# Kernel optimization log

Measured on AMD Instinct MI355X. Metric: run time of the kernel, lower is better.

The kernel has to match this reference:

```python
import jax, jax.numpy as jnp
import numpy as np

B, T, H, W = 32, 20, 64, 64
EPS = 1e-08
SPARSITY_W, CONC_W, FOCAL_ALPHA, COORD_W, BG_W = 0.8, 1.5, 1.0, 1.0, 0.1
GAMMA = 2.0


def setup_inputs() -> dict:
    key = jax.random.key(0)
    k1, k2 = jax.random.split(key)
    predictions = jax.random.normal(k1, (B, T, H, W), dtype=jnp.float32)
    targets = (jax.random.uniform(k2, (B, T, H, W)) < 0.001).astype(jnp.float32)
    return {"predictions": predictions, "targets": targets}


def _loss(pred, tgt):
    p = jax.nn.sigmoid(pred)                       # sigmoid computed once
    # focal loss (stable BCE-with-logits)
    bce = jnp.maximum(pred, 0.0) - pred * tgt + jnp.log1p(jnp.exp(-jnp.abs(pred)))
    p_t = jnp.where(tgt == 1.0, p, 1.0 - p)
    focal = jnp.mean(FOCAL_ALPHA * (1.0 - p_t) ** GAMMA * bce)
    # sparsity: entropy of per-(b,t) normalized map
    pf = p.reshape(B, T, H * W)
    pf_n = pf / (pf.sum(axis=-1, keepdims=True) + EPS)
    sparsity = jnp.mean(-jnp.sum(pf_n * jnp.log(pf_n + EPS), axis=-1))
    # concentration: 1 - max per (b,t)
    concentration = jnp.mean(1.0 - pf.max(axis=-1))
    # soft coordinate loss: center-of-mass distance per (b,t), fully vectorized
    xc = jnp.arange(W, dtype=jnp.float32)
    yc = jnp.arange(H, dtype=jnp.float32)
    ps = p.sum(axis=(-2, -1)) + EPS                 # [B,T]
    ts = tgt.sum(axis=(-2, -1)) + EPS
    px = jnp.einsum('bthw,w->bt', p, xc) / ps
    py = jnp.einsum('bthw,h->bt', p, yc) / ps
    tx = jnp.einsum('bthw,w->bt', tgt, xc) / ts
    ty = jnp.einsum('bthw,h->bt', tgt, yc) / ts
    coordinate = jnp.mean(jnp.sqrt((px - tx) ** 2 + (py - ty) ** 2))
    # background MSE
    background = jnp.mean((p * (tgt == 0.0).astype(p.dtype)) ** 2)
    total = (focal + SPARSITY_W * sparsity + CONC_W * concentration
             + COORD_W * coordinate + BG_W * background)
    return total


def reference(predictions, targets):
    return _loss(predictions, targets)
```

## Files before the change

kernel.cpp:

```cpp
#include <hip/hip_runtime.h>
#include <math.h>

#define B_ 32
#define T_ 20
#define H_ 64
#define W_ 64
#define HW 4096
#define BT 640
#define NTOT 2621440.0f
#define EPS 1e-8f
#define SPARSITY_W 0.8f
#define CONC_W 1.5f
#define COORD_W 1.0f
#define BG_W 0.1f

__global__ __launch_bounds__(256) void k1_stats(
    const float* __restrict__ pred, const float* __restrict__ tgt,
    float* __restrict__ stats)
{
    const int bt = blockIdx.x;
    const float4* p4 = (const float4*)(pred + (size_t)bt * HW);
    const float4* t4 = (const float4*)(tgt  + (size_t)bt * HW);

    float sp = 0.f, st = 0.f, spx = 0.f, spy = 0.f, stx = 0.f, sty = 0.f;
    float foc = 0.f, bg = 0.f, mx = -1e30f;

    for (int f = threadIdx.x; f < HW / 4; f += 256) {
        float4 xv = p4[f];
        float4 tv = t4[f];
        const int pix0 = f * 4;
        const float h  = (float)(pix0 >> 6);
        const float w0 = (float)(pix0 & 63);
        float xs[4] = {xv.x, xv.y, xv.z, xv.w};
        float ts[4] = {tv.x, tv.y, tv.z, tv.w};
#pragma unroll
        for (int k = 0; k < 4; k++) {
            const float x = xs[k];
            const float t = ts[k];
            const float p = 1.f / (1.f + expf(-x));
            const float bce = fmaxf(x, 0.f) - x * t + log1pf(expf(-fabsf(x)));
            const float pt = (t == 1.f) ? p : (1.f - p);
            const float om = 1.f - pt;
            foc += om * om * bce;
            if (t == 0.f) bg += p * p;
            const float w = w0 + (float)k;
            sp  += p;      st  += t;
            spx += p * w;  spy += p * h;
            stx += t * w;  sty += t * h;
            mx = fmaxf(mx, p);
        }
    }

    float vals[9] = {sp, st, spx, spy, stx, sty, foc, bg, mx};
#pragma unroll
    for (int o = 32; o > 0; o >>= 1) {
#pragma unroll
        for (int i = 0; i < 8; i++) vals[i] += __shfl_down(vals[i], o);
        vals[8] = fmaxf(vals[8], __shfl_down(vals[8], o));
    }
    __shared__ float sm[4][9];
    const int lane = threadIdx.x & 63;
    const int wv   = threadIdx.x >> 6;
    if (lane == 0) {
#pragma unroll
        for (int i = 0; i < 9; i++) sm[wv][i] = vals[i];
    }
    __syncthreads();
    if (threadIdx.x == 0) {
        float r[9];
#pragma unroll
        for (int i = 0; i < 9; i++) r[i] = sm[0][i];
        for (int v = 1; v < 4; v++) {
#pragma unroll
            for (int i = 0; i < 8; i++) r[i] += sm[v][i];
            r[8] = fmaxf(r[8], sm[v][8]);
        }
        const float Sp = r[0], St = r[1];
        const float psd = Sp + EPS, tsd = St + EPS;
        const float px = r[2] / psd, py = r[3] / psd;
        const float tx = r[4] / tsd, ty = r[5] / tsd;
        const float dx = px - tx, dy = py - ty;
        const float coord = sqrtf(dx * dx + dy * dy);
        const float contrib =
            r[6] * (1.0f / NTOT)
          + BG_W * r[7] * (1.0f / NTOT)
          + (CONC_W * (1.0f - r[8]) + COORD_W * coord) * (1.0f / (float)BT);
        stats[bt * 2 + 0] = contrib;
        stats[bt * 2 + 1] = Sp;
    }
}

__global__ __launch_bounds__(256) void k2_entropy(
    const float* __restrict__ pred, const float* __restrict__ stats,
    float* __restrict__ out)
{
    const int bt = blockIdx.x;
    const float Sp  = stats[bt * 2 + 1];
    const float inv = 1.f / (Sp + EPS);
    const float4* p4 = (const float4*)(pred + (size_t)bt * HW);

    float ent = 0.f;
    for (int f = threadIdx.x; f < HW / 4; f += 256) {
        float4 xv = p4[f];
        float xs[4] = {xv.x, xv.y, xv.z, xv.w};
#pragma unroll
        for (int k = 0; k < 4; k++) {
            const float p = 1.f / (1.f + expf(-xs[k]));
            const float q = p * inv;
            ent -= q * logf(q + EPS);
        }
    }
#pragma unroll
    for (int o = 32; o > 0; o >>= 1) ent += __shfl_down(ent, o);
    __shared__ float sm[4];
    const int lane = threadIdx.x & 63;
    const int wv   = threadIdx.x >> 6;
    if (lane == 0) sm[wv] = ent;
    __syncthreads();
    if (threadIdx.x == 0) {
        const float e = sm[0] + sm[1] + sm[2] + sm[3];
        atomicAdd(out, stats[bt * 2 + 0] + SPARSITY_W * e * (1.0f / (float)BT));
    }
}

extern "C" void kernel_launch(void* const* d_in, const int* in_sizes, int n_in,
                              void* d_out, int out_size, void* d_ws, size_t ws_size,
                              hipStream_t stream) {
    const float* pred = (const float*)d_in[0];
    const float* tgt  = (const float*)d_in[1];
    float* out   = (float*)d_out;
    float* stats = (float*)d_ws;

    hipMemsetAsync(out, 0, sizeof(float), stream);
    k1_stats<<<BT, 256, 0, stream>>>(pred, tgt, stats);
    k2_entropy<<<BT, 256, 0, stream>>>(pred, stats, out);
}
```

Baseline: 92.56 us.

## Fuse entropy pass into stats kernel via algebraic entropy decomposition

```diff
diff --git a/kernel.cpp b/kernel.cpp
--- a/kernel.cpp
+++ b/kernel.cpp
@@ -1,10 +1,6 @@
 #include <hip/hip_runtime.h>
 #include <math.h>
 
-#define B_ 32
-#define T_ 20
-#define H_ 64
-#define W_ 64
 #define HW 4096
 #define BT 640
 #define NTOT 2621440.0f
@@ -14,18 +10,20 @@
 #define COORD_W 1.0f
 #define BG_W 0.1f
 
-__global__ __launch_bounds__(256) void k1_stats(
+__global__ __launch_bounds__(256) void fused_loss(
     const float* __restrict__ pred, const float* __restrict__ tgt,
-    float* __restrict__ stats)
+    float* __restrict__ out)
 {
     const int bt = blockIdx.x;
     const float4* p4 = (const float4*)(pred + (size_t)bt * HW);
     const float4* t4 = (const float4*)(tgt  + (size_t)bt * HW);
 
     float sp = 0.f, st = 0.f, spx = 0.f, spy = 0.f, stx = 0.f, sty = 0.f;
-    float foc = 0.f, bg = 0.f, mx = -1e30f;
+    float foc = 0.f, bg = 0.f, splogp = 0.f, mx = -1e30f;
 
-    for (int f = threadIdx.x; f < HW / 4; f += 256) {
+#pragma unroll
+    for (int it = 0; it < 4; it++) {
+        const int f = threadIdx.x + it * 256;
         float4 xv = p4[f];
         float4 tv = t4[f];
         const int pix0 = f * 4;
@@ -43,6 +41,7 @@
             const float om = 1.f - pt;
             foc += om * om * bce;
             if (t == 0.f) bg += p * p;
+            splogp += p * logf(fmaxf(p, 1e-35f));
             const float w = w0 + (float)k;
             sp  += p;      st  += t;
             spx += p * w;  spy += p * h;
@@ -51,29 +50,29 @@
         }
     }
 
-    float vals[9] = {sp, st, spx, spy, stx, sty, foc, bg, mx};
+    float vals[10] = {sp, st, spx, spy, stx, sty, foc, bg, splogp, mx};
 #pragma unroll
     for (int o = 32; o > 0; o >>= 1) {
 #pragma unroll
-        for (int i = 0; i < 8; i++) vals[i] += __shfl_down(vals[i], o);
-        vals[8] = fmaxf(vals[8], __shfl_down(vals[8], o));
+        for (int i = 0; i < 9; i++) vals[i] += __shfl_down(vals[i], o);
+        vals[9] = fmaxf(vals[9], __shfl_down(vals[9], o));
     }
-    __shared__ float sm[4][9];
+    __shared__ float sm[4][10];
     const int lane = threadIdx.x & 63;
     const int wv   = threadIdx.x >> 6;
     if (lane == 0) {
 #pragma unroll
-        for (int i = 0; i < 9; i++) sm[wv][i] = vals[i];
+        for (int i = 0; i < 10; i++) sm[wv][i] = vals[i];
     }
     __syncthreads();
     if (threadIdx.x == 0) {
-        float r[9];
+        float r[10];
 #pragma unroll
-        for (int i = 0; i < 9; i++) r[i] = sm[0][i];
+        for (int i = 0; i < 10; i++) r[i] = sm[0][i];
         for (int v = 1; v < 4; v++) {
 #pragma unroll
-            for (int i = 0; i < 8; i++) r[i] += sm[v][i];
-            r[8] = fmaxf(r[8], sm[v][8]);
+            for (int i = 0; i < 9; i++) r[i] += sm[v][i];
+            r[9] = fmaxf(r[9], sm[v][9]);
         }
         const float Sp = r[0], St = r[1];
         const float psd = Sp + EPS, tsd = St + EPS;
@@ -81,45 +80,14 @@
         const float tx = r[4] / tsd, ty = r[5] / tsd;
         const float dx = px - tx, dy = py - ty;
         const float coord = sqrtf(dx * dx + dy * dy);
+        const float inv = 1.f / psd;
+        const float ent = -inv * r[8] - inv * Sp * logf(inv);
         const float contrib =
             r[6] * (1.0f / NTOT)
           + BG_W * r[7] * (1.0f / NTOT)
-          + (CONC_W * (1.0f - r[8]) + COORD_W * coord) * (1.0f / (float)BT);
-        stats[bt * 2 + 0] = contrib;
-        stats[bt * 2 + 1] = Sp;
-    }
-}
-
-__global__ __launch_bounds__(256) void k2_entropy(
-    const float* __restrict__ pred, const float* __restrict__ stats,
-    float* __restrict__ out)
-{
-    const int bt = blockIdx.x;
-    const float Sp  = stats[bt * 2 + 1];
-    const float inv = 1.f / (Sp + EPS);
-    const float4* p4 = (const float4*)(pred + (size_t)bt * HW);
-
-    float ent = 0.f;
-    for (int f = threadIdx.x; f < HW / 4; f += 256) {
-        float4 xv = p4[f];
-        float xs[4] = {xv.x, xv.y, xv.z, xv.w};
-#pragma unroll
-        for (int k = 0; k < 4; k++) {
-            const float p = 1.f / (1.f + expf(-xs[k]));
-            const float q = p * inv;
-            ent -= q * logf(q + EPS);
-        }
-    }
-#pragma unroll
-    for (int o = 32; o > 0; o >>= 1) ent += __shfl_down(ent, o);
-    __shared__ float sm[4];
-    const int lane = threadIdx.x & 63;
-    const int wv   = threadIdx.x >> 6;
-    if (lane == 0) sm[wv] = ent;
-    __syncthreads();
-    if (threadIdx.x == 0) {
-        const float e = sm[0] + sm[1] + sm[2] + sm[3];
-        atomicAdd(out, stats[bt * 2 + 0] + SPARSITY_W * e * (1.0f / (float)BT));
+          + (CONC_W * (1.0f - r[9]) + COORD_W * coord + SPARSITY_W * ent)
+                * (1.0f / (float)BT);
+        atomicAdd(out, contrib);
     }
 }
 
@@ -128,10 +96,8 @@
                               hipStream_t stream) {
     const float* pred = (const float*)d_in[0];
     const float* tgt  = (const float*)d_in[1];
-    float* out   = (float*)d_out;
-    float* stats = (float*)d_ws;
+    float* out = (float*)d_out;
 
     hipMemsetAsync(out, 0, sizeof(float), stream);
-    k1_stats<<<BT, 256, 0, stream>>>(pred, tgt, stats);
-    k2_entropy<<<BT, 256, 0, stream>>>(pred, stats, out);
+    fused_loss<<<BT, 256, 0, stream>>>(pred, tgt, out);
 }
```

Result: faster. 83.51 us (-9.8%).
